# Optimization experiments

Hardware: AMD Instinct MI355X
Metric: run time of the kernel (lower is better)

## Reference

```python
import jax, jax.numpy as jnp
import numpy as np
from jax import lax

DIST_THRESH = 180.0
ATT_THRESH = 0.05


def setup_inputs() -> dict:
    key = jax.random.key(0)
    ks = jax.random.split(key, 6)
    B, N, H, W = 16, 512, 25, 25
    F, Fh = H * W, int(H * W * 1.5)  # 625, 937
    x4 = jax.random.normal(ks[0], (B, N, H, W), dtype=jnp.float32) * 0.25
    attention = jax.random.uniform(ks[1], (B, N, 1, 1), dtype=jnp.float32)
    W1 = jax.random.normal(ks[2], (2, F, Fh), dtype=jnp.float32) * (1.0 / np.sqrt(F))
    b1 = jnp.zeros((Fh,), dtype=jnp.float32)
    W2 = jax.random.normal(ks[3], (2, Fh, F), dtype=jnp.float32) * (1.0 / np.sqrt(Fh))
    b2 = jnp.zeros((F,), dtype=jnp.float32)
    return {"x4": x4, "attention": attention, "W1": W1, "b1": b1, "W2": W2, "b2": b2}


def _build_adjacency(X, att):
    """X: [B,N,F] node features, att: [B,N]. Returns thresholded adjacency [B,N,N]."""
    B, N, F = X.shape
    # pairwise L1 distances, row-by-row scan to avoid materializing [B,N,N,F]
    Xs = jnp.swapaxes(X, 0, 1)  # [N,B,F]

    def row(_, xi):  # xi: [B,F]
        d = jnp.sum(jnp.abs(xi[:, None, :] - X), axis=-1)  # [B,N]
        return None, d

    _, D = lax.scan(row, None, Xs)          # [N,B,N]
    D = jnp.swapaxes(D, 0, 1)               # [B,N,N]
    att_d = jnp.abs(att[:, :, None] - att[:, None, :])  # [B,N,N]
    A = ((D <= DIST_THRESH) & (att_d <= ATT_THRESH)).astype(jnp.float32)
    # original only fills i<j and j<i, diagonal stays 0
    A = A * (1.0 - jnp.eye(N, dtype=jnp.float32))
    return A


def _process_graph(A):
    """A + I, then row-normalize by inverse degree (D^-1 (A+I))."""
    N = A.shape[1]
    A = A + jnp.eye(N, dtype=A.dtype)
    deg = jnp.sum(A, axis=-1)               # [B,N]
    dinv = jnp.where(deg > 0, 1.0 / deg, 0.0)
    return dinv[:, :, None] * A


def _cheb_conv(x, L, Wk, b):
    """ChebConv with K=2 over dense normalized graph L: T0=x, T1=Lx."""
    t1 = jnp.einsum('bij,bjf->bif', L, x)
    return jnp.einsum('bnf,fo->bno', x, Wk[0]) + jnp.einsum('bnf,fo->bno', t1, Wk[1]) + b


def reference(x4, attention, W1, b1, W2, b2):
    B, N, H, W = x4.shape
    X = x4.reshape(B, N, H * W)             # [B,N,625] flow_x
    att = attention[:, :, 0, 0]             # [B,N]
    A = _build_adjacency(X, att)
    L = _process_graph(A)
    h = jax.nn.relu(_cheb_conv(X, L, W1, b1))   # [B,N,937]
    out = jax.nn.relu(_cheb_conv(h, L, W2, b2))  # [B,N,625]
    return out
```

## Files before the change

kernel.cpp:

```cpp
#include <hip/hip_runtime.h>
#include <stdint.h>

typedef uint16_t u16;
typedef uint32_t u32;
typedef __attribute__((ext_vector_type(4))) float f32x4;
typedef __attribute__((ext_vector_type(4))) unsigned short us4;

#define NB   16
#define NN   512
#define FF   625
#define FH   937
#define ROWS 8192
#define KS1  1280
#define KS2  1920
#define NPX  640
#define NPH  960
#define F4   160
#define ITILE 4

using frag_ab = __attribute__((ext_vector_type(8))) short;
using frag_cd = __attribute__((ext_vector_type(4))) float;

__device__ __forceinline__ u16 f32_bf16(float f) {
  union { float f; uint32_t u; } x; x.f = f;
  uint32_t r = x.u + 0x7fffu + ((x.u >> 16) & 1u);
  return (u16)(r >> 16);
}
__device__ __forceinline__ void gload_lds16(const void* g, void* l) {
  __builtin_amdgcn_global_load_lds((__attribute__((address_space(1))) void*)g,
                                   (__attribute__((address_space(3))) void*)l,
                                   16, 0, 0);
}

__global__ __launch_bounds__(256) void prep(
    const float* __restrict__ x4, const float* __restrict__ att,
    const float* __restrict__ W1, const float* __restrict__ W2,
    f32x4* __restrict__ Xpad, u16* __restrict__ Xcat, u16* __restrict__ Xt,
    u16* __restrict__ W1t, u16* __restrict__ W2t,
    float* __restrict__ att_s, u16* __restrict__ ord_g)
{
  const int blk = blockIdx.x;
  const int tid = threadIdx.x;
  if (blk < 5120) {
    __shared__ float tile[32][33];
    const int xcd = blk & 7, sub = blk >> 3;
    const int b = xcd * 2 + sub / 320;
    const int t = sub % 320;
    const int ft = t % 20, kt = t / 20;
    const int tx = tid & 31, ty = tid >> 5;
    #pragma unroll
    for (int r = 0; r < 4; ++r) {
      const int node = kt * 32 + ty + r * 8;
      const int f = ft * 32 + tx;
      tile[ty + r * 8][tx] = (f < FF) ? x4[((size_t)b * NN + node) * FF + f] : 0.f;
    }
    __syncthreads();
    #pragma unroll
    for (int r = 0; r < 4; ++r) {
      const int f = ft * 32 + ty + r * 8;
      const int node = kt * 32 + tx;
      Xt[((size_t)b * NPX + f) * 512 + node] = f32_bf16(tile[tx][ty + r * 8]);
    }
    const int nd = tid >> 3, sl = tid & 7;
    const int row = b * NN + kt * 32 + nd;
    f32x4 v; us4 o;
    #pragma unroll
    for (int t2 = 0; t2 < 4; ++t2) {
      const float x = tile[nd][sl * 4 + t2];
      v[t2] = x; o[t2] = f32_bf16(x);
    }
    Xpad[(size_t)row * F4 + ft * 8 + sl] = v;
    *(us4*)(Xcat + (size_t)row * KS1 + ft * 32 + sl * 4) = o;
  } else if (blk < 6400) {
    __shared__ float tile[32][33];
    const int bb = blk - 5120;
    const int kt = bb % 40, nt = bb / 40;
    const int tx = tid & 31, ty = tid >> 5;
    #pragma unroll
    for (int r = 0; r < 4; ++r) {
      int k = kt * 32 + ty + r * 8;
      int n = nt * 32 + tx;
      float v = 0.f;
      int c = -1, kk = 0;
      if (k < 625) { c = 0; kk = k; }
      else if (k >= 640 && k < 1265) { c = 1; kk = k - 640; }
      if (c >= 0 && n < FH) v = W1[((size_t)c * 625 + kk) * FH + n];
      tile[ty + r * 8][tx] = v;
    }
    __syncthreads();
    #pragma unroll
    for (int r = 0; r < 4; ++r) {
      int n = nt * 32 + ty + r * 8;
      int k = kt * 32 + tx;
      W1t[(size_t)n * KS1 + k] = f32_bf16(tile[tx][ty + r * 8]);
    }
  } else if (blk < 7600) {
    __shared__ float tile[32][33];
    const int bb = blk - 6400;
    const int kt = bb % 60, nt = bb / 60;
    const int tx = tid & 31, ty = tid >> 5;
    #pragma unroll
    for (int r = 0; r < 4; ++r) {
      int k = kt * 32 + ty + r * 8;
      int n = nt * 32 + tx;
      float v = 0.f;
      int c = -1, kk = 0;
      if (k < 937) { c = 0; kk = k; }
      else if (k >= 960 && k < 1897) { c = 1; kk = k - 960; }
      if (c >= 0 && n < FF) v = W2[((size_t)c * 937 + kk) * FF + n];
      tile[ty + r * 8][tx] = v;
    }
    __syncthreads();
    #pragma unroll
    for (int r = 0; r < 4; ++r) {
      int n = nt * 32 + ty + r * 8;
      int k = kt * 32 + tx;
      W2t[(size_t)n * KS2 + k] = f32_bf16(tile[tx][ty + r * 8]);
    }
  } else {
    __shared__ float sa[512];
    __shared__ u16 so[512];
    const int b = blk - 7600;
    sa[tid] = att[b * NN + tid]; sa[tid + 256] = att[b * NN + tid + 256];
    so[tid] = (u16)tid; so[tid + 256] = (u16)(tid + 256);
    for (int k = 2; k <= 512; k <<= 1) {
      for (int j = k >> 1; j > 0; j >>= 1) {
        __syncthreads();
        const int i = ((tid & ~(j - 1)) << 1) | (tid & (j - 1));
        const int p = i | j;
        const bool up = ((i & k) == 0);
        const float va = sa[i], vp = sa[p];
        if ((va > vp) == up) {
          sa[i] = vp; sa[p] = va;
          const u16 t = so[i]; so[i] = so[p]; so[p] = t;
        }
      }
    }
    __syncthreads();
    att_s[b * NN + tid] = sa[tid]; att_s[b * NN + tid + 256] = sa[tid + 256];
    ord_g[b * NN + tid] = so[tid]; ord_g[b * NN + tid + 256] = so[tid + 256];
  }
}

__global__ __launch_bounds__(256) void build_L_tiled(
    const f32x4* __restrict__ Xpad,
    const float* __restrict__ att_s, const u16* __restrict__ ord_g,
    u16* __restrict__ L)
{
  __shared__ f32x4 Xi[ITILE][F4];
  __shared__ float as_[512];
  __shared__ u16 ord[512];
  __shared__ u16 inv[512];
  __shared__ u32 mask[ITILE][16];
  __shared__ int deg[ITILE];
  __shared__ int jlo_s, jhi_s;

  const int tid = threadIdx.x;
  const int blk = blockIdx.x;
  const int xcd = blk & 7, sub = blk >> 3;
  const int b = xcd * 2 + (sub >> 7);
  const int it = sub & 127;
  const int s0 = it * ITILE;
  const f32x4* Xb4 = Xpad + (size_t)b * NN * F4;

  as_[tid] = att_s[b * NN + tid]; as_[tid + 256] = att_s[b * NN + tid + 256];
  const u16 o0 = ord_g[b * NN + tid], o1 = ord_g[b * NN + tid + 256];
  ord[tid] = o0; ord[tid + 256] = o1;
  inv[o0] = (u16)tid; inv[o1] = (u16)(tid + 256);
  if (tid < ITILE * 16) ((u32*)mask)[tid] = 0;
  if (tid < ITILE) deg[tid] = 0;
  __syncthreads();

  for (int s = tid; s < ITILE * F4; s += 256) {
    const int ii = s / F4, k4 = s - ii * F4;
    Xi[ii][k4] = Xb4[(size_t)ord[s0 + ii] * F4 + k4];
  }
  if (tid == 0) {
    const float lot = as_[s0] - 0.05f;
    int lo = 0, hi = 512;
    while (lo < hi) { int m = (lo + hi) >> 1; if (as_[m] < lot) lo = m + 1; else hi = m; }
    jlo_s = lo;
  } else if (tid == 1) {
    const float hit = as_[s0 + ITILE - 1] + 0.05f;
    int lo = 0, hi = 512;
    while (lo < hi) { int m = (lo + hi) >> 1; if (as_[m] <= hit) lo = m + 1; else hi = m; }
    jhi_s = lo;
  }
  __syncthreads();

  const int hl = tid & 31;
  const int hw = tid >> 5;
  const int jlo = jlo_s, jhi = jhi_s;

  for (int sj = jlo + hw; sj < jhi; sj += 8) {
    const f32x4* Xj = Xb4 + (size_t)ord[sj] * F4;
    const f32x4 xj0 = Xj[hl];
    const f32x4 xj1 = Xj[32 + hl];
    const f32x4 xj2 = Xj[64 + hl];
    const f32x4 xj3 = Xj[96 + hl];
    const f32x4 xj4 = Xj[128 + hl];
    const float aj = as_[sj];
    f32x4 pv;
    #pragma unroll
    for (int ii = 0; ii < ITILE; ++ii) {
      const f32x4 d0 = Xi[ii][hl] - xj0;
      const f32x4 d1 = Xi[ii][32 + hl] - xj1;
      const f32x4 d2 = Xi[ii][64 + hl] - xj2;
      const f32x4 d3 = Xi[ii][96 + hl] - xj3;
      const f32x4 d4 = Xi[ii][128 + hl] - xj4;
      float p = 0.f;
      #pragma unroll
      for (int t = 0; t < 4; ++t)
        p += fabsf(d0[t]) + fabsf(d1[t]) + fabsf(d2[t]) + fabsf(d3[t]) + fabsf(d4[t]);
      pv[ii] = p;
    }
    #pragma unroll
    for (int off = 16; off; off >>= 1) {
      f32x4 o;
      o[0] = __shfl_xor(pv[0], off, 64);
      o[1] = __shfl_xor(pv[1], off, 64);
      o[2] = __shfl_xor(pv[2], off, 64);
      o[3] = __shfl_xor(pv[3], off, 64);
      pv += o;
    }
    if (hl == 0) {
      #pragma unroll
      for (int ii = 0; ii < ITILE; ++ii) {
        const int si = s0 + ii;
        if (si != sj && fabsf(aj - as_[si]) <= 0.05f && pv[ii] <= 180.0f) {
          atomicOr(&mask[ii][sj >> 5], 1u << (sj & 31));
          atomicAdd(&deg[ii], 1);
        }
      }
    }
  }
  __syncthreads();

  #pragma unroll
  for (int ii = 0; ii < ITILE; ++ii) {
    const int oi = ord[s0 + ii];
    const u16 dv = f32_bf16(1.0f / (float)(deg[ii] + 1));
    u16* Lrow = L + ((size_t)b * 512 + oi) * 512;
    const int j0 = 2 * tid;
    const int sA = inv[j0], sB = inv[j0 + 1];
    const u32 fA = (j0 == oi)     | ((mask[ii][sA >> 5] >> (sA & 31)) & 1u);
    const u32 fB = (j0 + 1 == oi) | ((mask[ii][sB >> 5] >> (sB & 31)) & 1u);
    *(u32*)(Lrow + j0) = (fA ? (u32)dv : 0u) | ((fB ? (u32)dv : 0u) << 16);
  }
}

template <int KS, int NTILE, int NREAL, int NSTORE, bool RELU, bool BIAS, bool OUT_BF16>
__device__ __forceinline__ void gemm_core(
    const u16* __restrict__ At, const u16* __restrict__ Btt,
    const float* __restrict__ bias, void* __restrict__ C,
    long crow0, int col0, int ldc)
{
  constexpr int NI = NTILE / 32;
  constexpr int BR = NTILE / 32;
  __shared__ __align__(16) u16 Ash[128 * 64];
  __shared__ __align__(16) u16 Bsh[NTILE * 64];

  const int tid  = threadIdx.x;
  const int lane = tid & 63;
  const int wave = tid >> 6;
  const int wm = wave & 1, wn = wave >> 1;
  const int q = lane >> 4, l16 = lane & 15;

  const u16* pa[4]; const u16* pb[BR];
  #pragma unroll
  for (int r = 0; r < 4; ++r) {
    const int ci = r * 256 + tid;
    const int row = ci >> 3, cpos = ci & 7;
    pa[r] = At + (size_t)row * KS + (cpos ^ (row & 7)) * 8;
  }
  #pragma unroll
  for (int r = 0; r < BR; ++r) {
    const int ci = r * 256 + tid;
    const int row = ci >> 3, cpos = ci & 7;
    pb[r] = Btt + (size_t)row * KS + (cpos ^ (row & 7)) * 8;
  }
  const int wbase = (tid & 192) * 8;

  const frag_ab* fA[4][2]; const frag_ab* fB[NI][2];
  #pragma unroll
  for (int mi = 0; mi < 4; ++mi) {
    const int row = wm * 64 + mi * 16 + l16;
    fA[mi][0] = (const frag_ab*)&Ash[row * 64 + ((q    ) ^ (l16 & 7)) * 8];
    fA[mi][1] = (const frag_ab*)&Ash[row * 64 + ((q + 4) ^ (l16 & 7)) * 8];
  }
  #pragma unroll
  for (int ni = 0; ni < NI; ++ni) {
    const int row = wn * (NTILE / 2) + ni * 16 + l16;
    fB[ni][0] = (const frag_ab*)&Bsh[row * 64 + ((q    ) ^ (l16 & 7)) * 8];
    fB[ni][1] = (const frag_ab*)&Bsh[row * 64 + ((q + 4) ^ (l16 & 7)) * 8];
  }

  frag_cd acc[4][NI] = {};

  constexpr int KT = KS / 64;
  for (int kt = 0; kt < KT; ++kt) {
    __syncthreads();
    #pragma unroll
    for (int r = 0; r < 4; ++r) { gload_lds16(pa[r], &Ash[r * 2048 + wbase]); pa[r] += 64; }
    #pragma unroll
    for (int r = 0; r < BR; ++r) { gload_lds16(pb[r], &Bsh[r * 2048 + wbase]); pb[r] += 64; }
    __syncthreads();

    #pragma unroll
    for (int kk = 0; kk < 2; ++kk) {
      frag_ab av[4], bv[NI];
      #pragma unroll
      for (int mi = 0; mi < 4; ++mi) av[mi] = *fA[mi][kk];
      #pragma unroll
      for (int ni = 0; ni < NI; ++ni) bv[ni] = *fB[ni][kk];
      #pragma unroll
      for (int mi = 0; mi < 4; ++mi)
        #pragma unroll
        for (int ni = 0; ni < NI; ++ni)
          acc[mi][ni] = __builtin_amdgcn_mfma_f32_16x16x32_bf16(
              av[mi], bv[ni], acc[mi][ni], 0, 0, 0);
    }
  }

  #pragma unroll
  for (int ni = 0; ni < NI; ++ni) {
    const int col = col0 + wn * (NTILE / 2) + ni * 16 + l16;
    if (col >= NSTORE) continue;
    const bool ok = (col < NREAL);
    float bvv = 0.f;
    if (BIAS) bvv = ok ? bias[col] : 0.f;
    #pragma unroll
    for (int mi = 0; mi < 4; ++mi) {
      #pragma unroll
      for (int r = 0; r < 4; ++r) {
        const long rowg = crow0 + wm * 64 + mi * 16 + q * 4 + r;
        float v = acc[mi][ni][r];
        if (BIAS) v += bvv;
        if (RELU) v = fmaxf(v, 0.f);
        if (!ok) v = 0.f;
        if (OUT_BF16) ((u16*)C)[rowg * (size_t)ldc + col] = f32_bf16(v);
        else          ((float*)C)[rowg * (size_t)ldc + col] = v;
      }
    }
  }
}

template <int KS, int NTILE, int NREAL, int NSTORE, bool RELU, bool BIAS, bool OUT_BF16>
__global__ __launch_bounds__(256) void gemm_dense(
    const u16* __restrict__ A, const u16* __restrict__ Bt,
    const float* __restrict__ bias, void* __restrict__ C, int ldc)
{
  const int x = blockIdx.x;
  const int mt = ((x & 7) << 3) | (x >> 3);
  gemm_core<KS, NTILE, NREAL, NSTORE, RELU, BIAS, OUT_BF16>(
      A + (size_t)mt * 128 * KS, Bt + (size_t)blockIdx.y * NTILE * KS,
      bias, C, (long)mt * 128, blockIdx.y * NTILE, ldc);
}

template <int NP>
__global__ __launch_bounds__(256) void spmm(
    const u16* __restrict__ L, const u16* __restrict__ Bt,
    u16* __restrict__ C, int ldc)
{
  constexpr int TPB = 4 * (NP / 64);
  const int blk = blockIdx.x;
  const int xcd = blk & 7, sub = blk >> 3;
  const int b = xcd * 2 + sub / TPB;
  const int t = sub % TPB;
  const int mt = t & 3, nt = t >> 2;
  gemm_core<512, 64, NP, NP, false, false, true>(
      L + ((size_t)b * 512 + mt * 128) * 512,
      Bt + ((size_t)b * NP + nt * 64) * 512,
      nullptr, C, (long)b * 512 + mt * 128, nt * 64, ldc);
}

__global__ __launch_bounds__(256) void transpose_h(
    const u16* __restrict__ hcat, u16* __restrict__ ht)
{
  __shared__ u16 tile[32][34];
  const int blk = blockIdx.x;
  const int xcd = blk & 7, sub = blk >> 3;
  const int b = xcd * 2 + sub / 480;
  const int t = sub % 480;
  const int kt = t % 16, nt = t / 16;
  const int tid = threadIdx.x;
  const int tx = tid & 31, ty = tid >> 5;
  #pragma unroll
  for (int r = 0; r < 4; ++r) {
    const int node = kt * 32 + ty + r * 8;
    const int n = nt * 32 + tx;
    tile[ty + r * 8][tx] = hcat[((size_t)b * NN + node) * KS2 + n];
  }
  __syncthreads();
  #pragma unroll
  for (int r = 0; r < 4; ++r) {
    const int n = nt * 32 + ty + r * 8;
    const int node = kt * 32 + tx;
    ht[((size_t)b * NPH + n) * 512 + node] = tile[tx][ty + r * 8];
  }
}

extern "C" void kernel_launch(void* const* d_in, const int* in_sizes, int n_in,
                              void* d_out, int out_size, void* d_ws, size_t ws_size,
                              hipStream_t stream) {
  const float* x4  = (const float*)d_in[0];
  const float* att = (const float*)d_in[1];
  const float* W1  = (const float*)d_in[2];
  const float* b1  = (const float*)d_in[3];
  const float* W2  = (const float*)d_in[4];
  const float* b2  = (const float*)d_in[5];
  float* out = (float*)d_out;

  char* ws = (char*)d_ws;
  f32x4* Xpad = (f32x4*)ws;
  u16* ht = (u16*)ws;       ws += (size_t)ROWS * F4 * 16;
  u16* Xcat = (u16*)ws;  ws += (size_t)ROWS * KS1 * 2;
  u16* hcat = (u16*)ws;  ws += (size_t)ROWS * KS2 * 2;
  u16* W1t  = (u16*)ws;  ws += (size_t)1024 * KS1 * 2;
  u16* W2t  = (u16*)ws;  ws += (size_t)640 * KS2 * 2;
  u16* Lm   = (u16*)ws;  ws += (size_t)NB * 512 * 512 * 2;
  u16* Xt   = (u16*)ws;  ws += (size_t)NB * NPX * 512 * 2;
  float* att_s = (float*)ws; ws += (size_t)NB * NN * 4;
  u16* ord_g   = (u16*)ws;   ws += (size_t)NB * NN * 2;

  prep<<<dim3(7616), 256, 0, stream>>>(x4, att, W1, W2, Xpad, Xcat, Xt,
                                       W1t, W2t, att_s, ord_g);
  build_L_tiled<<<dim3(2048), 256, 0, stream>>>(Xpad, att_s, ord_g, Lm);
  spmm<NPX><<<dim3(640), 256, 0, stream>>>(Lm, Xt, Xcat + NPX, KS1);
  gemm_dense<KS1, 128, FH, NPH, true, true, true>
      <<<dim3(64, 8), 256, 0, stream>>>(Xcat, W1t, b1, (void*)hcat, KS2);
  transpose_h<<<dim3(7680), 256, 0, stream>>>(hcat, ht);
  spmm<NPH><<<dim3(960), 256, 0, stream>>>(Lm, ht, hcat + NPH, KS2);
  gemm_dense<KS2, 64, FF, FF, true, true, false>
      <<<dim3(64, 10), 256, 0, stream>>>(hcat, W2t, b2, (void*)out, FF);
}
```

Baseline: 229.8 us.

## Exploit distance symmetry: compute upper triangle only, write adjacency bitmask globally

The adjacency build now evaluates only pairs with sj > si in sorted-attention order and sets both symmetric bits in a global bitmask with atomics, roughly halving the L1 distance work. Each wave now covers a full 64-lane feature row instead of a half-wave, and a new write_L kernel computes degrees by popcount and writes the bf16 normalized L. It adds an extra kernel launch, mask zeroing in prep, and global atomics. It also leaves some load imbalance, since blocks near the end of the sorted order have fewer pairs.

```diff
diff --git a/kernel.cpp b/kernel.cpp
--- a/kernel.cpp
+++ b/kernel.cpp
@@ -37,7 +37,7 @@
     const float* __restrict__ W1, const float* __restrict__ W2,
     f32x4* __restrict__ Xpad, u16* __restrict__ Xcat, u16* __restrict__ Xt,
     u16* __restrict__ W1t, u16* __restrict__ W2t,
-    float* __restrict__ att_s, u16* __restrict__ ord_g)
+    float* __restrict__ att_s, u16* __restrict__ ord_g, u32* __restrict__ gmask)
 {
   const int blk = blockIdx.x;
   const int tid = threadIdx.x;
@@ -121,6 +121,8 @@
     __shared__ float sa[512];
     __shared__ u16 so[512];
     const int b = blk - 7600;
+    u32* gm = gmask + (size_t)b * 512 * 16;
+    for (int s = tid; s < 512 * 16; s += 256) gm[s] = 0;
     sa[tid] = att[b * NN + tid]; sa[tid + 256] = att[b * NN + tid + 256];
     so[tid] = (u16)tid; so[tid + 256] = (u16)(tid + 256);
     for (int k = 2; k <= 512; k <<= 1) {
@@ -142,33 +144,25 @@
   }
 }
 
-__global__ __launch_bounds__(256) void build_L_tiled(
+__global__ __launch_bounds__(256) void build_L3(
     const f32x4* __restrict__ Xpad,
     const float* __restrict__ att_s, const u16* __restrict__ ord_g,
-    u16* __restrict__ L)
+    u32* __restrict__ gmask)
 {
   __shared__ f32x4 Xi[ITILE][F4];
   __shared__ float as_[512];
   __shared__ u16 ord[512];
-  __shared__ u16 inv[512];
-  __shared__ u32 mask[ITILE][16];
-  __shared__ int deg[ITILE];
-  __shared__ int jlo_s, jhi_s;
+  __shared__ int jhi_s;
 
   const int tid = threadIdx.x;
   const int blk = blockIdx.x;
   const int xcd = blk & 7, sub = blk >> 3;
   const int b = xcd * 2 + (sub >> 7);
-  const int it = sub & 127;
-  const int s0 = it * ITILE;
+  const int s0 = (sub & 127) * ITILE;
   const f32x4* Xb4 = Xpad + (size_t)b * NN * F4;
 
   as_[tid] = att_s[b * NN + tid]; as_[tid + 256] = att_s[b * NN + tid + 256];
-  const u16 o0 = ord_g[b * NN + tid], o1 = ord_g[b * NN + tid + 256];
-  ord[tid] = o0; ord[tid + 256] = o1;
-  inv[o0] = (u16)tid; inv[o1] = (u16)(tid + 256);
-  if (tid < ITILE * 16) ((u32*)mask)[tid] = 0;
-  if (tid < ITILE) deg[tid] = 0;
+  ord[tid] = ord_g[b * NN + tid]; ord[tid + 256] = ord_g[b * NN + tid + 256];
   __syncthreads();
 
   for (int s = tid; s < ITILE * F4; s += 256) {
@@ -176,11 +170,6 @@
     Xi[ii][k4] = Xb4[(size_t)ord[s0 + ii] * F4 + k4];
   }
   if (tid == 0) {
-    const float lot = as_[s0] - 0.05f;
-    int lo = 0, hi = 512;
-    while (lo < hi) { int m = (lo + hi) >> 1; if (as_[m] < lot) lo = m + 1; else hi = m; }
-    jlo_s = lo;
-  } else if (tid == 1) {
     const float hit = as_[s0 + ITILE - 1] + 0.05f;
     int lo = 0, hi = 512;
     while (lo < hi) { int m = (lo + hi) >> 1; if (as_[m] <= hit) lo = m + 1; else hi = m; }
@@ -188,34 +177,32 @@
   }
   __syncthreads();
 
-  const int hl = tid & 31;
-  const int hw = tid >> 5;
-  const int jlo = jlo_s, jhi = jhi_s;
-
-  for (int sj = jlo + hw; sj < jhi; sj += 8) {
-    const f32x4* Xj = Xb4 + (size_t)ord[sj] * F4;
-    const f32x4 xj0 = Xj[hl];
-    const f32x4 xj1 = Xj[32 + hl];
-    const f32x4 xj2 = Xj[64 + hl];
-    const f32x4 xj3 = Xj[96 + hl];
-    const f32x4 xj4 = Xj[128 + hl];
+  const int lane = tid & 63;
+  const int wave = tid >> 6;
+  const int jhi = jhi_s;
+  const f32x4 zero = {0.f, 0.f, 0.f, 0.f};
+
+  for (int sj = s0 + 1 + wave; sj < jhi; sj += 4) {
+    const int oj = __builtin_amdgcn_readfirstlane((int)ord[sj]);
+    const f32x4* Xj = Xb4 + (size_t)oj * F4;
+    const f32x4 xj0 = Xj[lane];
+    const f32x4 xj1 = Xj[64 + lane];
+    const f32x4 xj2 = (lane < 32) ? Xj[128 + lane] : zero;
     const float aj = as_[sj];
     f32x4 pv;
     #pragma unroll
     for (int ii = 0; ii < ITILE; ++ii) {
-      const f32x4 d0 = Xi[ii][hl] - xj0;
-      const f32x4 d1 = Xi[ii][32 + hl] - xj1;
-      const f32x4 d2 = Xi[ii][64 + hl] - xj2;
-      const f32x4 d3 = Xi[ii][96 + hl] - xj3;
-      const f32x4 d4 = Xi[ii][128 + hl] - xj4;
+      const f32x4 d0 = Xi[ii][lane] - xj0;
+      const f32x4 d1 = Xi[ii][64 + lane] - xj1;
+      const f32x4 d2 = (lane < 32) ? (Xi[ii][128 + lane] - xj2) : zero;
       float p = 0.f;
       #pragma unroll
       for (int t = 0; t < 4; ++t)
-        p += fabsf(d0[t]) + fabsf(d1[t]) + fabsf(d2[t]) + fabsf(d3[t]) + fabsf(d4[t]);
+        p += fabsf(d0[t]) + fabsf(d1[t]) + fabsf(d2[t]);
       pv[ii] = p;
     }
     #pragma unroll
-    for (int off = 16; off; off >>= 1) {
+    for (int off = 32; off; off >>= 1) {
       f32x4 o;
       o[0] = __shfl_xor(pv[0], off, 64);
       o[1] = __shfl_xor(pv[1], off, 64);
@@ -223,29 +210,59 @@
       o[3] = __shfl_xor(pv[3], off, 64);
       pv += o;
     }
-    if (hl == 0) {
+    if (lane == 0) {
       #pragma unroll
       for (int ii = 0; ii < ITILE; ++ii) {
         const int si = s0 + ii;
-        if (si != sj && fabsf(aj - as_[si]) <= 0.05f && pv[ii] <= 180.0f) {
-          atomicOr(&mask[ii][sj >> 5], 1u << (sj & 31));
-          atomicAdd(&deg[ii], 1);
+        if (sj > si && fabsf(aj - as_[si]) <= 0.05f && pv[ii] <= 180.0f) {
+          atomicOr(&gmask[((size_t)b * 512 + si) * 16 + (sj >> 5)], 1u << (sj & 31));
+          atomicOr(&gmask[((size_t)b * 512 + sj) * 16 + (si >> 5)], 1u << (si & 31));
         }
       }
     }
   }
+}
+
+__global__ __launch_bounds__(256) void write_L(
+    const u32* __restrict__ gmask, const u16* __restrict__ ord_g,
+    u16* __restrict__ L)
+{
+  __shared__ u32 msk[16][16];
+  __shared__ u16 ord[512];
+  __shared__ u16 inv[512];
+  __shared__ u16 dvs[16];
+
+  const int tid = threadIdx.x;
+  const int blk = blockIdx.x;
+  const int xcd = blk & 7, sub = blk >> 3;
+  const int b = xcd * 2 + (sub >> 5);
+  const int s0 = (sub & 31) * 16;
+
+  const u16 o0 = ord_g[b * NN + tid], o1 = ord_g[b * NN + tid + 256];
+  ord[tid] = o0; ord[tid + 256] = o1;
+  inv[o0] = (u16)tid; inv[o1] = (u16)(tid + 256);
+  if (tid < 256) msk[tid >> 4][tid & 15] =
+      gmask[((size_t)b * 512 + s0 + (tid >> 4)) * 16 + (tid & 15)];
   __syncthreads();
 
-  #pragma unroll
-  for (int ii = 0; ii < ITILE; ++ii) {
+  if (tid < 16) {
+    int d = 0;
+    #pragma unroll
+    for (int w = 0; w < 16; ++w) d += __popc(msk[tid][w]);
+    dvs[tid] = f32_bf16(1.0f / (float)(d + 1));
+  }
+  __syncthreads();
+
+  #pragma unroll 4
+  for (int ii = 0; ii < 16; ++ii) {
     const int oi = ord[s0 + ii];
-    const u16 dv = f32_bf16(1.0f / (float)(deg[ii] + 1));
-    u16* Lrow = L + ((size_t)b * 512 + oi) * 512;
+    const u16 dv = dvs[ii];
     const int j0 = 2 * tid;
     const int sA = inv[j0], sB = inv[j0 + 1];
-    const u32 fA = (j0 == oi)     | ((mask[ii][sA >> 5] >> (sA & 31)) & 1u);
-    const u32 fB = (j0 + 1 == oi) | ((mask[ii][sB >> 5] >> (sB & 31)) & 1u);
-    *(u32*)(Lrow + j0) = (fA ? (u32)dv : 0u) | ((fB ? (u32)dv : 0u) << 16);
+    const u32 fA = (j0 == oi)     | ((msk[ii][sA >> 5] >> (sA & 31)) & 1u);
+    const u32 fB = (j0 + 1 == oi) | ((msk[ii][sB >> 5] >> (sB & 31)) & 1u);
+    *(u32*)(L + ((size_t)b * 512 + oi) * 512 + j0) =
+        (fA ? (u32)dv : 0u) | ((fB ? (u32)dv : 0u) << 16);
   }
 }
 
@@ -420,12 +437,14 @@
   u16* W2t  = (u16*)ws;  ws += (size_t)640 * KS2 * 2;
   u16* Lm   = (u16*)ws;  ws += (size_t)NB * 512 * 512 * 2;
   u16* Xt   = (u16*)ws;  ws += (size_t)NB * NPX * 512 * 2;
+  u32* gmask = (u32*)ws; ws += (size_t)ROWS * 16 * 4;
   float* att_s = (float*)ws; ws += (size_t)NB * NN * 4;
   u16* ord_g   = (u16*)ws;   ws += (size_t)NB * NN * 2;
 
   prep<<<dim3(7616), 256, 0, stream>>>(x4, att, W1, W2, Xpad, Xcat, Xt,
-                                       W1t, W2t, att_s, ord_g);
-  build_L_tiled<<<dim3(2048), 256, 0, stream>>>(Xpad, att_s, ord_g, Lm);
+                                       W1t, W2t, att_s, ord_g, gmask);
+  build_L3<<<dim3(2048), 256, 0, stream>>>(Xpad, att_s, ord_g, gmask);
+  write_L<<<dim3(512), 256, 0, stream>>>(gmask, ord_g, Lm);
   spmm<NPX><<<dim3(640), 256, 0, stream>>>(Lm, Xt, Xcat + NPX, KS1);
   gemm_dense<KS1, 128, FH, NPH, true, true, true>
       <<<dim3(64, 8), 256, 0, stream>>>(Xcat, W1t, b1, (void*)hcat, KS2);
```

New measurement: 222.9 us. 3.0% less time.
